# Kernel optimization log

Hardware: AMD Instinct MI355X
Metric: run time of the kernel (lower is better)

Reference implementation:

```python
import jax, jax.numpy as jnp
import numpy as np

N_NODES = 50000
N_GRAPHS = 32
NODE_F = 16
GLOBAL_F = 2
HID = 300
LAT = 100
N_EDGES = 800000


def _glorot(key, shape):
    fan_in, fan_out = shape[0], shape[1]
    s = jnp.sqrt(2.0 / (fan_in + fan_out))
    return jax.random.normal(key, shape, dtype=jnp.float32) * s


def setup_inputs() -> dict:
    key = jax.random.key(0)
    ks = jax.random.split(key, 24)
    x = jax.random.normal(ks[0], (N_NODES, NODE_F), dtype=jnp.float32)
    edge_index = jax.random.randint(ks[1], (2, N_EDGES), 0, N_NODES, dtype=jnp.int64)
    batch = jnp.sort(jax.random.randint(ks[2], (N_NODES,), 0, N_GRAPHS, dtype=jnp.int64))
    u = jax.random.normal(ks[3], (N_GRAPHS, GLOBAL_F), dtype=jnp.float32)
    # layer 0: in=NODE_F, layer 1: in=LAT
    p = {}
    p['l0_w1'] = _glorot(ks[4], (2 * NODE_F, HID)); p['l0_b1'] = jnp.zeros((HID,), jnp.float32)
    p['l0_w2'] = _glorot(ks[5], (HID, HID));        p['l0_b2'] = jnp.zeros((HID,), jnp.float32)
    p['l0_w3'] = _glorot(ks[6], (HID, LAT));        p['l0_b3'] = jnp.zeros((LAT,), jnp.float32)
    p['l1_w1'] = _glorot(ks[7], (2 * LAT, HID));    p['l1_b1'] = jnp.zeros((HID,), jnp.float32)
    p['l1_w2'] = _glorot(ks[8], (HID, HID));        p['l1_b2'] = jnp.zeros((HID,), jnp.float32)
    p['l1_w3'] = _glorot(ks[9], (HID, LAT));        p['l1_b3'] = jnp.zeros((LAT,), jnp.float32)
    p['lin_w1'] = _glorot(ks[10], (LAT + GLOBAL_F, LAT)); p['lin_b1'] = jnp.zeros((LAT,), jnp.float32)
    p['lin_w2'] = _glorot(ks[11], (LAT, LAT));            p['lin_b2'] = jnp.zeros((LAT,), jnp.float32)
    p['lin_w3'] = _glorot(ks[12], (LAT, 1));              p['lin_b3'] = jnp.zeros((1,), jnp.float32)
    return dict(x=x, edge_index=edge_index, batch=batch, u=u, **p)


def _edge_layer(x, src, dst, w1, b1, w2, b2, w3, b3):
    # gather endpoints; torch_geometric default flow: x_j = x[src], x_i = x[dst]
    xi = x[dst]
    xj = x[src]
    inp = jnp.concatenate([xi, xj - xi], axis=-1)          # [E, 2*in]
    h = jax.nn.relu(inp @ w1 + b1)
    h = jax.nn.relu(h @ w2 + b2)
    m = h @ w3 + b3                                         # [E, out]
    s = jax.ops.segment_sum(m, dst, num_segments=N_NODES)  # scatter-sum to target nodes
    cnt = jax.ops.segment_sum(jnp.ones((m.shape[0],), m.dtype), dst, num_segments=N_NODES)
    return s / jnp.maximum(cnt, 1.0)[:, None]               # scatter-mean


def _mean_pool(x, batch):
    s = jax.ops.segment_sum(x, batch, num_segments=N_GRAPHS)
    cnt = jax.ops.segment_sum(jnp.ones((x.shape[0],), x.dtype), batch, num_segments=N_GRAPHS)
    return s / jnp.maximum(cnt, 1.0)[:, None]


def reference(x, edge_index, batch, u,
              l0_w1, l0_b1, l0_w2, l0_b2, l0_w3, l0_b3,
              l1_w1, l1_b1, l1_w2, l1_b2, l1_w3, l1_b3,
              lin_w1, lin_b1, lin_w2, lin_b2, lin_w3, lin_b3):
    src, dst = edge_index[0], edge_index[1]
    x = _edge_layer(x, src, dst, l0_w1, l0_b1, l0_w2, l0_b2, l0_w3, l0_b3)
    x = jax.nn.relu(x)
    x = _edge_layer(x, src, dst, l1_w1, l1_b1, l1_w2, l1_b2, l1_w3, l1_b3)
    x = jax.nn.relu(x)
    pooled = jnp.concatenate([_mean_pool(x, batch), u], axis=1)  # [G, LAT+GLOBAL_F]
    h = jax.nn.relu(pooled @ lin_w1 + lin_b1)
    h = jax.nn.relu(h @ lin_w2 + lin_b2)
    return h @ lin_w3 + lin_b3  # [G, 1]
```

## Files before the change

### kernel.cpp

```cpp
#include <hip/hip_runtime.h>
#include <cstdint>
#include <cstddef>

#define N_NODES  50000
#define N_GRAPHS 32
#define NODE_F   16
#define GLOBAL_F 2
#define HID      300
#define LAT      100
#define N_EDGES  800000

#define HIDP 320
#define LATP 128
#define NCT1 (HIDP/16)
#define NCT2 (LATP/16)
#define NKS  (HIDP/32)
#define EPB  64
#define NTILE 12500
#define HSFS 132

#define W2F_ELEMS 102400
#define W3F_ELEMS 40960
#define W1F0_ELEMS 20480
#define W1F1_ELEMS 81920

typedef __bf16 bf16x8 __attribute__((ext_vector_type(8)));
typedef float  f32x4  __attribute__((ext_vector_type(4)));

__device__ __forceinline__ float relu_f(float x){ return fmaxf(x, 0.f); }

__device__ __forceinline__ unsigned short f2bf(float x){
  unsigned int u = __float_as_uint(x);
  u = (u + 0x7FFFu + ((u >> 16) & 1u)) >> 16;
  return (unsigned short)u;
}
__device__ __forceinline__ unsigned short f2bf_hw(float x){
  __bf16 h = (__bf16)x;
  return __builtin_bit_cast(unsigned short, h);
}
__device__ __forceinline__ float bf2f(unsigned int h){
  return __uint_as_float(h << 16);
}

__device__ __forceinline__ void pack_one(const float* __restrict__ w, int K, int N,
                                         int nct, unsigned short* __restrict__ out, int i){
  int j  = i & 7;
  int l  = (i >> 3) & 63;
  int t  = i >> 9;
  int ct = t % nct, ks = t / nct;
  int n = ct*16 + (l & 15);
  int k = ks*32 + ((l >> 4) << 3) + j;
  float v = (k < K && n < N) ? w[(size_t)k*N + n] : 0.f;
  out[i] = f2bf(v);
}

__device__ __forceinline__ void pack_w1_one(const float* __restrict__ w1, int F,
                                            unsigned short* __restrict__ out, int i){
  int j  = i & 7;
  int l  = (i >> 3) & 63;
  int t  = i >> 9;
  int ct = t % 40, ks = t / 40;
  int n = ct*16 + (l & 15);
  int k = ks*32 + ((l >> 4) << 3) + j;
  float v = 0.f;
  if (k < F){
    if (n < HIDP){ if (n < HID) v = w1[(size_t)k*HID + n] - w1[(size_t)(F+k)*HID + n]; }
    else { int nn = n - HIDP; if (nn < HID) v = w1[(size_t)(F+k)*HID + nn]; }
  }
  out[i] = f2bf(v);
}

#define PR_B0 (2*N_NODES*LAT + N_NODES)
#define PR_B1 (PR_B0 + 2*W2F_ELEMS + 2*W3F_ELEMS)
#define PR_B2 (PR_B1 + W1F0_ELEMS)
#define PR_B3 (PR_B2 + W1F1_ELEMS)
#define PR_B4 (PR_B3 + HIDP)
#define PR_B5 (PR_B4 + N_NODES*32)

__global__ void prep_kernel(
    int* __restrict__ zero_region,
    const float* __restrict__ w2a, const float* __restrict__ w3a,
    const float* __restrict__ w2b, const float* __restrict__ w3b,
    unsigned short* __restrict__ o2a, unsigned short* __restrict__ o3a,
    unsigned short* __restrict__ o2b, unsigned short* __restrict__ o3b,
    const float* __restrict__ w1a, unsigned short* __restrict__ o1a,
    const float* __restrict__ w1b, unsigned short* __restrict__ o1b,
    const float* __restrict__ ba0, const float* __restrict__ ba1,
    const float* __restrict__ ba2, const float* __restrict__ ba3,
    float* __restrict__ bo0, float* __restrict__ bo1,
    float* __restrict__ bo2, float* __restrict__ bo3,
    const float* __restrict__ x, unsigned short* __restrict__ xb){
  int i = blockIdx.x*blockDim.x + threadIdx.x;
  if (i < PR_B0){ zero_region[i] = 0; return; }
  if (i < PR_B1){
    int t = i - PR_B0;
    if (t < W2F_ELEMS) pack_one(w2a, HID, HID, NCT1, o2a, t);
    else if (t < W2F_ELEMS + W3F_ELEMS) pack_one(w3a, HID, LAT, NCT2, o3a, t - W2F_ELEMS);
    else if (t < 2*W2F_ELEMS + W3F_ELEMS) pack_one(w2b, HID, HID, NCT1, o2b, t - W2F_ELEMS - W3F_ELEMS);
    else pack_one(w3b, HID, LAT, NCT2, o3b, t - 2*W2F_ELEMS - W3F_ELEMS);
    return;
  }
  if (i < PR_B2){ pack_w1_one(w1a, NODE_F, o1a, i - PR_B1); return; }
  if (i < PR_B3){ pack_w1_one(w1b, LAT,    o1b, i - PR_B2); return; }
  if (i < PR_B4){
    int t = i - PR_B3;
    bo0[t] = (t < HID) ? ba0[t] : 0.f;
    bo1[t] = (t < HID) ? ba1[t] : 0.f;
    bo2[t] = (t < HID) ? ba2[t] : 0.f;
    bo3[t] = (t < HID) ? ba3[t] : 0.f;
    return;
  }
  if (i < PR_B5){
    int t = i - PR_B4;
    int n = t >> 5, c = t & 31;
    xb[t] = (c < NODE_F) ? f2bf(x[(size_t)n*NODE_F + c]) : 0;
    return;
  }
}

__global__ void hist_kernel(const int* __restrict__ ei, int* __restrict__ hist){
  int e = blockIdx.x*blockDim.x + threadIdx.x;
  if (e < N_EDGES) atomicAdd(&hist[ei[N_EDGES + e]], 1);
}

__global__ __launch_bounds__(256) void scan_kernel(const int* __restrict__ hist,
                                                   int* __restrict__ woff){
  __shared__ int part[256];
  const int t = threadIdx.x;
  const int CH = (N_NODES + 255) / 256;
  const int lo = t*CH, hi = (lo + CH < N_NODES) ? lo + CH : N_NODES;
  int s = 0;
  for (int i = lo; i < hi; ++i) s += hist[i];
  part[t] = s;
  __syncthreads();
  for (int d = 1; d < 256; d <<= 1){
    int v = (t >= d) ? part[t-d] : 0;
    __syncthreads();
    part[t] += v;
    __syncthreads();
  }
  int run = (t == 0) ? 0 : part[t-1];
  for (int i = lo; i < hi; ++i){ woff[i] = run; run += hist[i]; }
}

__global__ void sort_gstart(const int* __restrict__ ei, int* __restrict__ woff,
                            int2* __restrict__ esd,
                            const int* __restrict__ batch, int* __restrict__ gstart){
  int e = blockIdx.x*blockDim.x + threadIdx.x;
  if (e < N_EDGES){
    int s = ei[e], d = ei[N_EDGES + e];
    int pos = atomicAdd(&woff[d], 1);
    esd[pos] = make_int2(s, d);
  }
  if (e < N_NODES){
    int n = e;
    int b = batch[n];
    if (n == 0){ for (int g = 0; g <= b; ++g) gstart[g] = 0; }
    else {
      int bp = batch[n-1];
      for (int g = bp+1; g <= b; ++g) gstart[g] = n;
    }
    if (n == N_NODES-1){ for (int g = b+1; g <= N_GRAPHS; ++g) gstart[g] = N_NODES; }
  }
}

__global__ __launch_bounds__(256) void node_gemm0(
    const unsigned short* __restrict__ xb, const unsigned short* __restrict__ wf,
    const float* __restrict__ b1p,
    unsigned short* __restrict__ Ub, unsigned short* __restrict__ Vb){
  constexpr int KPAD = 32, NCH = KPAD/8;
  __shared__ __align__(16) unsigned short at[NCH][66][8];
  const int tid = threadIdx.x;
  const int n0 = blockIdx.x*64;
  for (int i = tid; i < 64*NCH; i += 256){
    int row = i / NCH, c = i % NCH;
    int n = n0 + row; if (n >= N_NODES) n = N_NODES-1;
    *(uint4*)&at[c][row][0] = *(const uint4*)&xb[(size_t)n*KPAD + c*8];
  }
  __syncthreads();
  const int wave = tid >> 6, l = tid & 63;
  const int lrow = l & 15, lq = l >> 4;
  f32x4 acc[4][10];
  #pragma unroll
  for (int rt = 0; rt < 4; ++rt)
    #pragma unroll
    for (int c = 0; c < 10; ++c)
      acc[rt][c] = (f32x4){0.f,0.f,0.f,0.f};
  for (int ks = 0; ks < KPAD/32; ++ks){
    bf16x8 a[4];
    #pragma unroll
    for (int rt = 0; rt < 4; ++rt)
      a[rt] = __builtin_bit_cast(bf16x8, *(const uint4*)&at[4*ks + lq][16*rt + lrow][0]);
    #pragma unroll
    for (int c = 0; c < 10; ++c){
      int ct = wave*10 + c;
      bf16x8 b = __builtin_bit_cast(bf16x8,
                   *(const uint4*)&wf[(((size_t)(ks*40 + ct)) << 9) + l*8]);
      #pragma unroll
      for (int rt = 0; rt < 4; ++rt)
        acc[rt][c] = __builtin_amdgcn_mfma_f32_16x16x32_bf16(a[rt], b, acc[rt][c], 0, 0, 0);
    }
  }
  #pragma unroll
  for (int c = 0; c < 10; ++c){
    int col = (wave*10 + c)*16 + lrow;
    const bool isU = (col < HIDP);
    const float bv = isU ? b1p[col] : 0.f;
    #pragma unroll
    for (int rt = 0; rt < 4; ++rt){
      #pragma unroll
      for (int r = 0; r < 4; ++r){
        int n = n0 + rt*16 + lq*4 + r;
        if (n < N_NODES){
          if (isU) Ub[(size_t)n*HIDP + col] = f2bf_hw(acc[rt][c][r] + bv);
          else     Vb[(size_t)n*HIDP + col - HIDP] = f2bf_hw(acc[rt][c][r]);
        }
      }
    }
  }
}

__global__ __launch_bounds__(256) void node_gemm1(
    const float* __restrict__ nacc, const int* __restrict__ hist,
    const float* __restrict__ b3,
    const unsigned short* __restrict__ wf, const float* __restrict__ b1p,
    unsigned short* __restrict__ Ub, unsigned short* __restrict__ Vb){
  constexpr int KPAD = 128, NCH = KPAD/8;
  __shared__ __align__(16) unsigned short at[NCH][66][8];
  const int tid = threadIdx.x;
  const int n0 = blockIdx.x*64;
  for (int i = tid; i < 64*NCH; i += 256){
    int row = i >> 4, c = i & 15;
    int n = n0 + row; if (n >= N_NODES) n = N_NODES-1;
    unsigned short o[8];
    if (c < 13){
      int cnt = hist[n];
      float inv = 1.f / fmaxf((float)cnt, 1.f);
      float4 a = *(const float4*)&nacc[(size_t)n*LAT + c*8];
      float4 b = (c < 12) ? *(const float4*)&nacc[(size_t)n*LAT + c*8 + 4]
                          : make_float4(0.f,0.f,0.f,0.f);
      float vals[8] = {a.x,a.y,a.z,a.w,b.x,b.y,b.z,b.w};
      #pragma unroll
      for (int q = 0; q < 8; ++q){
        int col = c*8 + q;
        float v = 0.f;
        if (col < LAT){
          v = vals[q]*inv + ((cnt > 0) ? b3[col] : 0.f);
          v = relu_f(v);
        }
        o[q] = f2bf_hw(v);
      }
    } else {
      #pragma unroll
      for (int q = 0; q < 8; ++q) o[q] = 0;
    }
    *(uint4*)&at[c][row][0] = *(const uint4*)o;
  }
  __syncthreads();
  const int wave = tid >> 6, l = tid & 63;
  const int lrow = l & 15, lq = l >> 4;
  f32x4 acc[4][10];
  #pragma unroll
  for (int rt = 0; rt < 4; ++rt)
    #pragma unroll
    for (int c = 0; c < 10; ++c)
      acc[rt][c] = (f32x4){0.f,0.f,0.f,0.f};
  for (int ks = 0; ks < KPAD/32; ++ks){
    bf16x8 a[4];
    #pragma unroll
    for (int rt = 0; rt < 4; ++rt)
      a[rt] = __builtin_bit_cast(bf16x8, *(const uint4*)&at[4*ks + lq][16*rt + lrow][0]);
    #pragma unroll
    for (int c = 0; c < 10; ++c){
      int ct = wave*10 + c;
      bf16x8 b = __builtin_bit_cast(bf16x8,
                   *(const uint4*)&wf[(((size_t)(ks*40 + ct)) << 9) + l*8]);
      #pragma unroll
      for (int rt = 0; rt < 4; ++rt)
        acc[rt][c] = __builtin_amdgcn_mfma_f32_16x16x32_bf16(a[rt], b, acc[rt][c], 0, 0, 0);
    }
  }
  #pragma unroll
  for (int c = 0; c < 10; ++c){
    int col = (wave*10 + c)*16 + lrow;
    const bool isU = (col < HIDP);
    const float bv = isU ? b1p[col] : 0.f;
    #pragma unroll
    for (int rt = 0; rt < 4; ++rt){
      #pragma unroll
      for (int r = 0; r < 4; ++r){
        int n = n0 + rt*16 + lq*4 + r;
        if (n < N_NODES){
          if (isU) Ub[(size_t)n*HIDP + col] = f2bf_hw(acc[rt][c][r] + bv);
          else     Vb[(size_t)n*HIDP + col - HIDP] = f2bf_hw(acc[rt][c][r]);
        }
      }
    }
  }
}

__global__ __launch_bounds__(256, 3) void edge_mfma(
    const int2* __restrict__ esd,
    const unsigned short* __restrict__ U, const unsigned short* __restrict__ V,
    const unsigned short* __restrict__ w2f,
    const float* __restrict__ b2p, const unsigned short* __restrict__ w3f,
    float* __restrict__ nodeacc){
  __shared__ __align__(16) unsigned short hsb[40*64*8];
  __shared__ int sdst[EPB];
  __shared__ int sflag[EPB];
  float* hsf = (float*)hsb;
  #define HS(c,row) (hsb + (((((c)<<6)) + (((row) ^ (((c)&3)<<2)))) << 3))

  const int tid = threadIdx.x;
  const int bid = blockIdx.x;
  const int rtile = (bid & 7)*1563 + (bid >> 3);
  if (rtile >= NTILE) return;
  const int e0 = rtile * EPB;
  const int eL = tid & 63;
  const int2 se = esd[e0 + eL];
  const int mysrc = se.x, mydst = se.y;
  if (tid < EPB) sdst[tid] = mydst;

  const size_t ub = (size_t)mydst*HIDP;
  const size_t vb = (size_t)mysrc*HIDP;
  const int c0 = tid >> 6;
  uint4 uu = *(const uint4*)&U[ub + c0*8];
  uint4 vv = *(const uint4*)&V[vb + c0*8];
  #pragma unroll
  for (int it = 0; it < 10; ++it){
    const int c = c0 + it*4;
    uint4 uun, vvn;
    if (it < 9){
      uun = *(const uint4*)&U[ub + (size_t)(c+4)*8];
      vvn = *(const uint4*)&V[vb + (size_t)(c+4)*8];
    }
    const unsigned int ua[4] = {uu.x,uu.y,uu.z,uu.w};
    const unsigned int va[4] = {vv.x,vv.y,vv.z,vv.w};
    unsigned int ou[4];
    #pragma unroll
    for (int q = 0; q < 4; ++q){
      float f0 = relu_f(bf2f(ua[q] & 0xFFFFu) + bf2f(va[q] & 0xFFFFu));
      float f1 = relu_f(bf2f(ua[q] >> 16)     + bf2f(va[q] >> 16));
      ou[q] = (unsigned int)f2bf_hw(f0) | ((unsigned int)f2bf_hw(f1) << 16);
    }
    *(uint4*)HS(c, eL) = make_uint4(ou[0], ou[1], ou[2], ou[3]);
    if (it < 9){ uu = uun; vv = vvn; }
  }
  __syncthreads();

  const int wave = tid >> 6, l = tid & 63;
  const int lrow = l & 15, lq = l >> 4;

  f32x4 acc1[4][5];
  #pragma unroll
  for (int rt = 0; rt < 4; ++rt)
    #pragma unroll
    for (int c = 0; c < 5; ++c)
      acc1[rt][c] = (f32x4){0.f,0.f,0.f,0.f};
  for (int ks = 0; ks < NKS; ++ks){
    bf16x8 a[4];
    #pragma unroll
    for (int rt = 0; rt < 4; ++rt)
      a[rt] = __builtin_bit_cast(bf16x8, *(const uint4*)HS(4*ks + lq, 16*rt + lrow));
    #pragma unroll
    for (int c = 0; c < 5; ++c){
      int ct = wave*5 + c;
      bf16x8 b = __builtin_bit_cast(bf16x8,
                   *(const uint4*)&w2f[(((size_t)(ks*NCT1 + ct)) << 9) + l*8]);
      #pragma unroll
      for (int rt = 0; rt < 4; ++rt)
        acc1[rt][c] = __builtin_amdgcn_mfma_f32_16x16x32_bf16(a[rt], b, acc1[rt][c], 0, 0, 0);
    }
  }
  __syncthreads();

  #pragma unroll
  for (int c = 0; c < 5; ++c){
    int col = (wave*5 + c)*16 + lrow;
    float b2v = b2p[col];
    #pragma unroll
    for (int rt = 0; rt < 4; ++rt){
      #pragma unroll
      for (int r = 0; r < 4; ++r){
        int row = rt*16 + lq*4 + r;
        HS(col >> 3, row)[col & 7] = f2bf_hw(relu_f(acc1[rt][c][r] + b2v));
      }
    }
  }
  __syncthreads();

  f32x4 acc2[4][2];
  #pragma unroll
  for (int rt = 0; rt < 4; ++rt)
    #pragma unroll
    for (int c = 0; c < 2; ++c)
      acc2[rt][c] = (f32x4){0.f,0.f,0.f,0.f};
  for (int ks = 0; ks < NKS; ++ks){
    bf16x8 a[4];
    #pragma unroll
    for (int rt = 0; rt < 4; ++rt)
      a[rt] = __builtin_bit_cast(bf16x8, *(const uint4*)HS(4*ks + lq, 16*rt + lrow));
    #pragma unroll
    for (int c = 0; c < 2; ++c){
      int ct = wave*2 + c;
      bf16x8 b = __builtin_bit_cast(bf16x8,
                   *(const uint4*)&w3f[(((size_t)(ks*NCT2 + ct)) << 9) + l*8]);
      #pragma unroll
      for (int rt = 0; rt < 4; ++rt)
        acc2[rt][c] = __builtin_amdgcn_mfma_f32_16x16x32_bf16(a[rt], b, acc2[rt][c], 0, 0, 0);
    }
  }
  __syncthreads();

  #pragma unroll
  for (int c = 0; c < 2; ++c){
    int col = (wave*2 + c)*16 + lrow;
    #pragma unroll
    for (int rt = 0; rt < 4; ++rt){
      #pragma unroll
      for (int r = 0; r < 4; ++r){
        int row = rt*16 + lq*4 + r;
        hsf[row*HSFS + col] = acc2[rt][c][r];
      }
    }
  }
  if (tid < EPB) sflag[tid] = (tid == 0) || (sdst[tid] != sdst[tid-1]);
  __syncthreads();

  {
    const int col = tid & 127;
    if (col < LAT){
      for (int s = tid >> 7; s < EPB; s += 2){
        if (!sflag[s]) continue;
        int d = sdst[s];
        float sum = hsf[s*HSFS + col];
        int r = s + 1;
        while (r < EPB && !sflag[r]){ sum += hsf[r*HSFS + col]; ++r; }
        atomicAdd(&nodeacc[(size_t)d*LAT + col], sum);
      }
    }
  }
  #undef HS
}

__global__ void finalize_kernel(const float* __restrict__ nodeacc,
                                const int* __restrict__ hist,
                                const float* __restrict__ b3,
                                unsigned short* __restrict__ x1b){
  int idx = blockIdx.x*blockDim.x + threadIdx.x;
  if (idx < N_NODES*128){
    int n = idx >> 7, j = idx & 127;
    unsigned short o = 0;
    if (j < LAT){
      int c = hist[n];
      float v = nodeacc[(size_t)n*LAT + j] / fmaxf((float)c, 1.f);
      v += (c > 0) ? b3[j] : 0.f;
      o = f2bf_hw(relu_f(v));
    }
    x1b[idx] = o;
  }
}

__global__ __launch_bounds__(1024) void pool_seg(const unsigned short* __restrict__ x1b,
                                                 const int* __restrict__ gstart,
                                                 float* __restrict__ pooled){
  __shared__ float buf[7][128];
  const int g = blockIdx.x;
  const int lo = gstart[g], hi = gstart[g+1];
  const int col = threadIdx.x & 127, q = threadIdx.x >> 7;
  float s = 0.f;
  for (int n = lo + q; n < hi; n += 8) s += bf2f(x1b[(size_t)n*128 + col]);
  if (q) buf[q-1][col] = s;
  __syncthreads();
  if (q == 0 && col < LAT){
    float tot = s;
    #pragma unroll
    for (int k = 0; k < 7; ++k) tot += buf[k][col];
    pooled[g*LAT + col] = tot / fmaxf((float)(hi - lo), 1.f);
  }
}

__global__ __launch_bounds__(128) void head_kernel(
    const float* __restrict__ pooled,
    const float* __restrict__ u,
    const float* __restrict__ w1, const float* __restrict__ bb1,
    const float* __restrict__ w2, const float* __restrict__ bb2,
    const float* __restrict__ w3, const float* __restrict__ bb3,
    float* __restrict__ out){
  __shared__ float p[N_GRAPHS][LAT+GLOBAL_F];
  __shared__ float h1[N_GRAPHS][LAT];
  __shared__ float h2[N_GRAPHS][LAT];
  const int tid = threadIdx.x;
  for (int t = tid; t < N_GRAPHS*LAT; t += 128){
    int g = t / LAT, k = t - g*LAT;
    p[g][k] = pooled[t];
  }
  for (int t = tid; t < N_GRAPHS*GLOBAL_F; t += 128){
    int g = t / GLOBAL_F, c = t - g*GLOBAL_F;
    p[g][LAT + c] = u[t];
  }
  __syncthreads();
  for (int t = tid; t < N_GRAPHS*LAT; t += 128){
    int g = t / LAT, j = t - g*LAT;
    float s = bb1[j];
    for (int k = 0; k < LAT+GLOBAL_F; k++) s += p[g][k]*w1[(size_t)k*LAT + j];
    h1[g][j] = relu_f(s);
  }
  __syncthreads();
  for (int t = tid; t < N_GRAPHS*LAT; t += 128){
    int g = t / LAT, j = t - g*LAT;
    float s = bb2[j];
    for (int k = 0; k < LAT; k++) s += h1[g][k]*w2[(size_t)k*LAT + j];
    h2[g][j] = relu_f(s);
  }
  __syncthreads();
  for (int t = tid; t < N_GRAPHS; t += 128){
    float s = bb3[0];
    for (int k = 0; k < LAT; k++) s += h2[t][k]*w3[k];
    out[t] = s;
  }
}

extern "C" void kernel_launch(void* const* d_in, const int* in_sizes, int n_in,
                              void* d_out, int out_size, void* d_ws, size_t ws_size,
                              hipStream_t stream){
  (void)in_sizes; (void)n_in; (void)out_size; (void)ws_size;
  const float* x     = (const float*)d_in[0];
  const int*   ei    = (const int*)d_in[1];
  const int*   batch = (const int*)d_in[2];
  const float* u     = (const float*)d_in[3];
  const float* l0_w1 = (const float*)d_in[4];  const float* l0_b1 = (const float*)d_in[5];
  const float* l0_w2 = (const float*)d_in[6];  const float* l0_b2 = (const float*)d_in[7];
  const float* l0_w3 = (const float*)d_in[8];  const float* l0_b3 = (const float*)d_in[9];
  const float* l1_w1 = (const float*)d_in[10]; const float* l1_b1 = (const float*)d_in[11];
  const float* l1_w2 = (const float*)d_in[12]; const float* l1_b2 = (const float*)d_in[13];
  const float* l1_w3 = (const float*)d_in[14]; const float* l1_b3 = (const float*)d_in[15];
  const float* lin_w1= (const float*)d_in[16]; const float* lin_b1= (const float*)d_in[17];
  const float* lin_w2= (const float*)d_in[18]; const float* lin_b2= (const float*)d_in[19];
  const float* lin_w3= (const float*)d_in[20]; const float* lin_b3= (const float*)d_in[21];

  char* wsb = (char*)d_ws;
  const size_t UV_BYTES = (size_t)N_NODES*HIDP*sizeof(unsigned short);

  unsigned short* Ub   = (unsigned short*)wsb;  wsb += UV_BYTES;
  unsigned short* Vb   = (unsigned short*)wsb;  wsb += UV_BYTES;
  unsigned short* w2f0 = (unsigned short*)wsb;  wsb += (size_t)W2F_ELEMS*2;
  unsigned short* w3f0 = (unsigned short*)wsb;  wsb += (size_t)W3F_ELEMS*2;
  unsigned short* w2f1 = (unsigned short*)wsb;  wsb += (size_t)W2F_ELEMS*2;
  unsigned short* w3f1 = (unsigned short*)wsb;  wsb += (size_t)W3F_ELEMS*2;
  unsigned short* w1f0 = (unsigned short*)wsb;  wsb += (size_t)W1F0_ELEMS*2;
  unsigned short* w1f1 = (unsigned short*)wsb;  wsb += (size_t)W1F1_ELEMS*2;
  float* b1p0 = (float*)wsb;                    wsb += HIDP*4;
  float* b2p0 = (float*)wsb;                    wsb += HIDP*4;
  float* b1p1 = (float*)wsb;                    wsb += HIDP*4;
  float* b2p1 = (float*)wsb;                    wsb += HIDP*4;
  unsigned short* xb0 = (unsigned short*)wsb;   wsb += (size_t)N_NODES*32*2;
  unsigned short* x1b = (unsigned short*)wsb;   wsb += (size_t)N_NODES*128*2;
  float* nodeaccA = (float*)wsb;                wsb += (size_t)N_NODES*LAT*4;
  float* nodeaccB = (float*)wsb;                wsb += (size_t)N_NODES*LAT*4;
  int*   hist    = (int*)wsb;                   wsb += (size_t)N_NODES*4;
  int*   woff    = (int*)wsb;                   wsb += (size_t)N_NODES*4;
  int2*  esd     = (int2*)wsb;                  wsb += (size_t)N_EDGES*8;
  int*   gstart  = (int*)wsb;                   wsb += 64*4;
  float* pooled  = (float*)wsb;                 wsb += (size_t)N_GRAPHS*LAT*4;

  hipLaunchKernelGGL(prep_kernel, dim3((PR_B5+255)/256), dim3(256), 0, stream,
                     (int*)nodeaccA,
                     l0_w2, l0_w3, l1_w2, l1_w3, w2f0, w3f0, w2f1, w3f1,
                     l0_w1, w1f0, l1_w1, w1f1,
                     l0_b1, l0_b2, l1_b1, l1_b2, b1p0, b2p0, b1p1, b2p1,
                     x, xb0);
  hipLaunchKernelGGL(hist_kernel, dim3((N_EDGES+255)/256), dim3(256), 0, stream, ei, hist);
  hipLaunchKernelGGL(scan_kernel, dim3(1), dim3(256), 0, stream, hist, woff);
  hipLaunchKernelGGL(sort_gstart, dim3((N_EDGES+255)/256), dim3(256), 0, stream,
                     ei, woff, esd, batch, gstart);

  const int NGB = (N_NODES + 63)/64;
  const int NEBP = 8*1563;

  hipLaunchKernelGGL(node_gemm0, dim3(NGB), dim3(256), 0, stream,
                     xb0, w1f0, b1p0, Ub, Vb);
  hipLaunchKernelGGL(edge_mfma, dim3(NEBP), dim3(256), 0, stream,
                     esd, Ub, Vb, w2f0, b2p0, w3f0, nodeaccA);

  hipLaunchKernelGGL(node_gemm1, dim3(NGB), dim3(256), 0, stream,
                     nodeaccA, hist, l0_b3, w1f1, b1p1, Ub, Vb);
  hipLaunchKernelGGL(edge_mfma, dim3(NEBP), dim3(256), 0, stream,
                     esd, Ub, Vb, w2f1, b2p1, w3f1, nodeaccB);
  hipLaunchKernelGGL(finalize_kernel, dim3((N_NODES*128+255)/256), dim3(256), 0, stream,
                     nodeaccB, hist, l1_b3, x1b);

  hipLaunchKernelGGL(pool_seg, dim3(N_GRAPHS), dim3(1024), 0, stream, x1b, gstart, pooled);
  hipLaunchKernelGGL(head_kernel, dim3(1), dim3(128), 0, stream,
                     pooled, u, lin_w1, lin_b1, lin_w2, lin_b2, lin_w3, lin_b3,
                     (float*)d_out);
}
```

Baseline: 1.558 ms.

## Switch bf16 MFMA path to fp16, reuse one node accumulator, simplify edge tiling

Moves all packed weights, activations and MFMA calls from bf16 to fp16. The edge prologue now does add and relu as packed half-vector ops instead of per-element unpack, convert and repack. The two node accumulator buffers become one, with node_gemm1 zeroing it after reading, which shrinks the prep zero-fill. The edge kernel drops its interleaved tile remap in favour of a plain blockIdx mapping. Using fp16 narrows the dynamic range of intermediates compared with bf16, and the plain mapping changes the order in which scatter atomics hit memory.

```diff
diff --git a/kernel.cpp b/kernel.cpp
--- a/kernel.cpp
+++ b/kernel.cpp
@@ -24,22 +24,17 @@
 #define W1F0_ELEMS 20480
 #define W1F1_ELEMS 81920
 
-typedef __bf16 bf16x8 __attribute__((ext_vector_type(8)));
-typedef float  f32x4  __attribute__((ext_vector_type(4)));
+typedef _Float16 f16x8 __attribute__((ext_vector_type(8)));
+typedef float    f32x4 __attribute__((ext_vector_type(4)));
 
 __device__ __forceinline__ float relu_f(float x){ return fmaxf(x, 0.f); }
 
-__device__ __forceinline__ unsigned short f2bf(float x){
-  unsigned int u = __float_as_uint(x);
-  u = (u + 0x7FFFu + ((u >> 16) & 1u)) >> 16;
-  return (unsigned short)u;
-}
-__device__ __forceinline__ unsigned short f2bf_hw(float x){
-  __bf16 h = (__bf16)x;
+__device__ __forceinline__ unsigned short f2h(float x){
+  _Float16 h = (_Float16)x;
   return __builtin_bit_cast(unsigned short, h);
 }
-__device__ __forceinline__ float bf2f(unsigned int h){
-  return __uint_as_float(h << 16);
+__device__ __forceinline__ float h2f(unsigned short v){
+  return (float)__builtin_bit_cast(_Float16, v);
 }
 
 __device__ __forceinline__ void pack_one(const float* __restrict__ w, int K, int N,
@@ -51,7 +46,7 @@
   int n = ct*16 + (l & 15);
   int k = ks*32 + ((l >> 4) << 3) + j;
   float v = (k < K && n < N) ? w[(size_t)k*N + n] : 0.f;
-  out[i] = f2bf(v);
+  out[i] = f2h(v);
 }
 
 __device__ __forceinline__ void pack_w1_one(const float* __restrict__ w1, int F,
@@ -67,10 +62,10 @@
     if (n < HIDP){ if (n < HID) v = w1[(size_t)k*HID + n] - w1[(size_t)(F+k)*HID + n]; }
     else { int nn = n - HIDP; if (nn < HID) v = w1[(size_t)(F+k)*HID + nn]; }
   }
-  out[i] = f2bf(v);
-}
-
-#define PR_B0 (2*N_NODES*LAT + N_NODES)
+  out[i] = f2h(v);
+}
+
+#define PR_B0 (N_NODES*LAT + N_NODES)
 #define PR_B1 (PR_B0 + 2*W2F_ELEMS + 2*W3F_ELEMS)
 #define PR_B2 (PR_B1 + W1F0_ELEMS)
 #define PR_B3 (PR_B2 + W1F1_ELEMS)
@@ -113,7 +108,7 @@
   if (i < PR_B5){
     int t = i - PR_B4;
     int n = t >> 5, c = t & 31;
-    xb[t] = (c < NODE_F) ? f2bf(x[(size_t)n*NODE_F + c]) : 0;
+    xb[t] = (c < NODE_F) ? f2h(x[(size_t)n*NODE_F + c]) : 0;
     return;
   }
 }
@@ -187,18 +182,18 @@
     for (int c = 0; c < 10; ++c)
       acc[rt][c] = (f32x4){0.f,0.f,0.f,0.f};
   for (int ks = 0; ks < KPAD/32; ++ks){
-    bf16x8 a[4];
+    f16x8 a[4];
     #pragma unroll
     for (int rt = 0; rt < 4; ++rt)
-      a[rt] = __builtin_bit_cast(bf16x8, *(const uint4*)&at[4*ks + lq][16*rt + lrow][0]);
+      a[rt] = __builtin_bit_cast(f16x8, *(const uint4*)&at[4*ks + lq][16*rt + lrow][0]);
     #pragma unroll
     for (int c = 0; c < 10; ++c){
       int ct = wave*10 + c;
-      bf16x8 b = __builtin_bit_cast(bf16x8,
+      f16x8 b = __builtin_bit_cast(f16x8,
                    *(const uint4*)&wf[(((size_t)(ks*40 + ct)) << 9) + l*8]);
       #pragma unroll
       for (int rt = 0; rt < 4; ++rt)
-        acc[rt][c] = __builtin_amdgcn_mfma_f32_16x16x32_bf16(a[rt], b, acc[rt][c], 0, 0, 0);
+        acc[rt][c] = __builtin_amdgcn_mfma_f32_16x16x32_f16(a[rt], b, acc[rt][c], 0, 0, 0);
     }
   }
   #pragma unroll
@@ -212,8 +207,8 @@
       for (int r = 0; r < 4; ++r){
         int n = n0 + rt*16 + lq*4 + r;
         if (n < N_NODES){
-          if (isU) Ub[(size_t)n*HIDP + col] = f2bf_hw(acc[rt][c][r] + bv);
-          else     Vb[(size_t)n*HIDP + col - HIDP] = f2bf_hw(acc[rt][c][r]);
+          if (isU) Ub[(size_t)n*HIDP + col] = f2h(acc[rt][c][r] + bv);
+          else     Vb[(size_t)n*HIDP + col - HIDP] = f2h(acc[rt][c][r]);
         }
       }
     }
@@ -221,7 +216,7 @@
 }
 
 __global__ __launch_bounds__(256) void node_gemm1(
-    const float* __restrict__ nacc, const int* __restrict__ hist,
+    float* __restrict__ nacc, const int* __restrict__ hist,
     const float* __restrict__ b3,
     const unsigned short* __restrict__ wf, const float* __restrict__ b1p,
     unsigned short* __restrict__ Ub, unsigned short* __restrict__ Vb){
@@ -231,11 +226,14 @@
   const int n0 = blockIdx.x*64;
   for (int i = tid; i < 64*NCH; i += 256){
     int row = i >> 4, c = i & 15;
-    int n = n0 + row; if (n >= N_NODES) n = N_NODES-1;
+    int nr = n0 + row;
+    const bool owner = (nr < N_NODES);
+    int n = owner ? nr : N_NODES-1;
     unsigned short o[8];
     if (c < 13){
       int cnt = hist[n];
       float inv = 1.f / fmaxf((float)cnt, 1.f);
+      float bsel = (cnt > 0) ? 1.f : 0.f;
       float4 a = *(const float4*)&nacc[(size_t)n*LAT + c*8];
       float4 b = (c < 12) ? *(const float4*)&nacc[(size_t)n*LAT + c*8 + 4]
                           : make_float4(0.f,0.f,0.f,0.f);
@@ -244,11 +242,12 @@
       for (int q = 0; q < 8; ++q){
         int col = c*8 + q;
         float v = 0.f;
-        if (col < LAT){
-          v = vals[q]*inv + ((cnt > 0) ? b3[col] : 0.f);
-          v = relu_f(v);
-        }
-        o[q] = f2bf_hw(v);
+        if (col < LAT) v = relu_f(vals[q]*inv + bsel*b3[col]);
+        o[q] = f2h(v);
+      }
+      if (owner){
+        *(float4*)&nacc[(size_t)n*LAT + c*8] = make_float4(0.f,0.f,0.f,0.f);
+        if (c < 12) *(float4*)&nacc[(size_t)n*LAT + c*8 + 4] = make_float4(0.f,0.f,0.f,0.f);
       }
     } else {
       #pragma unroll
@@ -266,18 +265,18 @@
     for (int c = 0; c < 10; ++c)
       acc[rt][c] = (f32x4){0.f,0.f,0.f,0.f};
   for (int ks = 0; ks < KPAD/32; ++ks){
-    bf16x8 a[4];
+    f16x8 a[4];
     #pragma unroll
     for (int rt = 0; rt < 4; ++rt)
-      a[rt] = __builtin_bit_cast(bf16x8, *(const uint4*)&at[4*ks + lq][16*rt + lrow][0]);
+      a[rt] = __builtin_bit_cast(f16x8, *(const uint4*)&at[4*ks + lq][16*rt + lrow][0]);
     #pragma unroll
     for (int c = 0; c < 10; ++c){
       int ct = wave*10 + c;
-      bf16x8 b = __builtin_bit_cast(bf16x8,
+      f16x8 b = __builtin_bit_cast(f16x8,
                    *(const uint4*)&wf[(((size_t)(ks*40 + ct)) << 9) + l*8]);
       #pragma unroll
       for (int rt = 0; rt < 4; ++rt)
-        acc[rt][c] = __builtin_amdgcn_mfma_f32_16x16x32_bf16(a[rt], b, acc[rt][c], 0, 0, 0);
+        acc[rt][c] = __builtin_amdgcn_mfma_f32_16x16x32_f16(a[rt], b, acc[rt][c], 0, 0, 0);
     }
   }
   #pragma unroll
@@ -291,8 +290,8 @@
       for (int r = 0; r < 4; ++r){
         int n = n0 + rt*16 + lq*4 + r;
         if (n < N_NODES){
-          if (isU) Ub[(size_t)n*HIDP + col] = f2bf_hw(acc[rt][c][r] + bv);
-          else     Vb[(size_t)n*HIDP + col - HIDP] = f2bf_hw(acc[rt][c][r]);
+          if (isU) Ub[(size_t)n*HIDP + col] = f2h(acc[rt][c][r] + bv);
+          else     Vb[(size_t)n*HIDP + col - HIDP] = f2h(acc[rt][c][r]);
         }
       }
     }
@@ -312,10 +311,7 @@
   #define HS(c,row) (hsb + (((((c)<<6)) + (((row) ^ (((c)&3)<<2)))) << 3))
 
   const int tid = threadIdx.x;
-  const int bid = blockIdx.x;
-  const int rtile = (bid & 7)*1563 + (bid >> 3);
-  if (rtile >= NTILE) return;
-  const int e0 = rtile * EPB;
+  const int e0 = blockIdx.x * EPB;
   const int eL = tid & 63;
   const int2 se = esd[e0 + eL];
   const int mysrc = se.x, mydst = se.y;
@@ -326,6 +322,7 @@
   const int c0 = tid >> 6;
   uint4 uu = *(const uint4*)&U[ub + c0*8];
   uint4 vv = *(const uint4*)&V[vb + c0*8];
+  const f16x8 zero8 = (f16x8)(_Float16)0.f;
   #pragma unroll
   for (int it = 0; it < 10; ++it){
     const int c = c0 + it*4;
@@ -334,16 +331,9 @@
       uun = *(const uint4*)&U[ub + (size_t)(c+4)*8];
       vvn = *(const uint4*)&V[vb + (size_t)(c+4)*8];
     }
-    const unsigned int ua[4] = {uu.x,uu.y,uu.z,uu.w};
-    const unsigned int va[4] = {vv.x,vv.y,vv.z,vv.w};
-    unsigned int ou[4];
-    #pragma unroll
-    for (int q = 0; q < 4; ++q){
-      float f0 = relu_f(bf2f(ua[q] & 0xFFFFu) + bf2f(va[q] & 0xFFFFu));
-      float f1 = relu_f(bf2f(ua[q] >> 16)     + bf2f(va[q] >> 16));
-      ou[q] = (unsigned int)f2bf_hw(f0) | ((unsigned int)f2bf_hw(f1) << 16);
-    }
-    *(uint4*)HS(c, eL) = make_uint4(ou[0], ou[1], ou[2], ou[3]);
+    f16x8 s = __builtin_bit_cast(f16x8, uu) + __builtin_bit_cast(f16x8, vv);
+    s = __builtin_elementwise_max(s, zero8);
+    *(uint4*)HS(c, eL) = __builtin_bit_cast(uint4, s);
     if (it < 9){ uu = uun; vv = vvn; }
   }
   __syncthreads();
@@ -358,18 +348,18 @@
     for (int c = 0; c < 5; ++c)
       acc1[rt][c] = (f32x4){0.f,0.f,0.f,0.f};
   for (int ks = 0; ks < NKS; ++ks){
-    bf16x8 a[4];
+    f16x8 a[4];
     #pragma unroll
     for (int rt = 0; rt < 4; ++rt)
-      a[rt] = __builtin_bit_cast(bf16x8, *(const uint4*)HS(4*ks + lq, 16*rt + lrow));
+      a[rt] = __builtin_bit_cast(f16x8, *(const uint4*)HS(4*ks + lq, 16*rt + lrow));
     #pragma unroll
     for (int c = 0; c < 5; ++c){
       int ct = wave*5 + c;
-      bf16x8 b = __builtin_bit_cast(bf16x8,
+      f16x8 b = __builtin_bit_cast(f16x8,
                    *(const uint4*)&w2f[(((size_t)(ks*NCT1 + ct)) << 9) + l*8]);
       #pragma unroll
       for (int rt = 0; rt < 4; ++rt)
-        acc1[rt][c] = __builtin_amdgcn_mfma_f32_16x16x32_bf16(a[rt], b, acc1[rt][c], 0, 0, 0);
+        acc1[rt][c] = __builtin_amdgcn_mfma_f32_16x16x32_f16(a[rt], b, acc1[rt][c], 0, 0, 0);
     }
   }
   __syncthreads();
@@ -383,7 +373,7 @@
       #pragma unroll
       for (int r = 0; r < 4; ++r){
         int row = rt*16 + lq*4 + r;
-        HS(col >> 3, row)[col & 7] = f2bf_hw(relu_f(acc1[rt][c][r] + b2v));
+        HS(col >> 3, row)[col & 7] = f2h(relu_f(acc1[rt][c][r] + b2v));
       }
     }
   }
@@ -396,18 +386,18 @@
     for (int c = 0; c < 2; ++c)
       acc2[rt][c] = (f32x4){0.f,0.f,0.f,0.f};
   for (int ks = 0; ks < NKS; ++ks){
-    bf16x8 a[4];
+    f16x8 a[4];
     #pragma unroll
     for (int rt = 0; rt < 4; ++rt)
-      a[rt] = __builtin_bit_cast(bf16x8, *(const uint4*)HS(4*ks + lq, 16*rt + lrow));
+      a[rt] = __builtin_bit_cast(f16x8, *(const uint4*)HS(4*ks + lq, 16*rt + lrow));
     #pragma unroll
     for (int c = 0; c < 2; ++c){
       int ct = wave*2 + c;
-      bf16x8 b = __builtin_bit_cast(bf16x8,
+      f16x8 b = __builtin_bit_cast(f16x8,
                    *(const uint4*)&w3f[(((size_t)(ks*NCT2 + ct)) << 9) + l*8]);
       #pragma unroll
       for (int rt = 0; rt < 4; ++rt)
-        acc2[rt][c] = __builtin_amdgcn_mfma_f32_16x16x32_bf16(a[rt], b, acc2[rt][c], 0, 0, 0);
+        acc2[rt][c] = __builtin_amdgcn_mfma_f32_16x16x32_f16(a[rt], b, acc2[rt][c], 0, 0, 0);
     }
   }
   __syncthreads();
@@ -455,7 +445,7 @@
       int c = hist[n];
       float v = nodeacc[(size_t)n*LAT + j] / fmaxf((float)c, 1.f);
       v += (c > 0) ? b3[j] : 0.f;
-      o = f2bf_hw(relu_f(v));
+      o = f2h(relu_f(v));
     }
     x1b[idx] = o;
   }
@@ -469,7 +459,7 @@
   const int lo = gstart[g], hi = gstart[g+1];
   const int col = threadIdx.x & 127, q = threadIdx.x >> 7;
   float s = 0.f;
-  for (int n = lo + q; n < hi; n += 8) s += bf2f(x1b[(size_t)n*128 + col]);
+  for (int n = lo + q; n < hi; n += 8) s += h2f(x1b[(size_t)n*128 + col]);
   if (q) buf[q-1][col] = s;
   __syncthreads();
   if (q == 0 && col < LAT){
@@ -556,8 +546,7 @@
   float* b2p1 = (float*)wsb;                    wsb += HIDP*4;
   unsigned short* xb0 = (unsigned short*)wsb;   wsb += (size_t)N_NODES*32*2;
   unsigned short* x1b = (unsigned short*)wsb;   wsb += (size_t)N_NODES*128*2;
-  float* nodeaccA = (float*)wsb;                wsb += (size_t)N_NODES*LAT*4;
-  float* nodeaccB = (float*)wsb;                wsb += (size_t)N_NODES*LAT*4;
+  float* nodeacc = (float*)wsb;                 wsb += (size_t)N_NODES*LAT*4;
   int*   hist    = (int*)wsb;                   wsb += (size_t)N_NODES*4;
   int*   woff    = (int*)wsb;                   wsb += (size_t)N_NODES*4;
   int2*  esd     = (int2*)wsb;                  wsb += (size_t)N_EDGES*8;
@@ -565,7 +554,7 @@
   float* pooled  = (float*)wsb;                 wsb += (size_t)N_GRAPHS*LAT*4;
 
   hipLaunchKernelGGL(prep_kernel, dim3((PR_B5+255)/256), dim3(256), 0, stream,
-                     (int*)nodeaccA,
+                     (int*)nodeacc,
                      l0_w2, l0_w3, l1_w2, l1_w3, w2f0, w3f0, w2f1, w3f1,
                      l0_w1, w1f0, l1_w1, w1f1,
                      l0_b1, l0_b2, l1_b1, l1_b2, b1p0, b2p0, b1p1, b2p1,
@@ -576,19 +565,18 @@
                      ei, woff, esd, batch, gstart);
 
   const int NGB = (N_NODES + 63)/64;
-  const int NEBP = 8*1563;
 
   hipLaunchKernelGGL(node_gemm0, dim3(NGB), dim3(256), 0, stream,
                      xb0, w1f0, b1p0, Ub, Vb);
-  hipLaunchKernelGGL(edge_mfma, dim3(NEBP), dim3(256), 0, stream,
-                     esd, Ub, Vb, w2f0, b2p0, w3f0, nodeaccA);
+  hipLaunchKernelGGL(edge_mfma, dim3(NTILE), dim3(256), 0, stream,
+                     esd, Ub, Vb, w2f0, b2p0, w3f0, nodeacc);
 
   hipLaunchKernelGGL(node_gemm1, dim3(NGB), dim3(256), 0, stream,
-                     nodeaccA, hist, l0_b3, w1f1, b1p1, Ub, Vb);
-  hipLaunchKernelGGL(edge_mfma, dim3(NEBP), dim3(256), 0, stream,
-                     esd, Ub, Vb, w2f1, b2p1, w3f1, nodeaccB);
+                     nodeacc, hist, l0_b3, w1f1, b1p1, Ub, Vb);
+  hipLaunchKernelGGL(edge_mfma, dim3(NTILE), dim3(256), 0, stream,
+                     esd, Ub, Vb, w2f1, b2p1, w3f1, nodeacc);
   hipLaunchKernelGGL(finalize_kernel, dim3((N_NODES*128+255)/256), dim3(256), 0, stream,
-                     nodeaccB, hist, l1_b3, x1b);
+                     nodeacc, hist, l1_b3, x1b);
 
   hipLaunchKernelGGL(pool_seg, dim3(N_GRAPHS), dim3(1024), 0, stream, x1b, gstart, pooled);
   hipLaunchKernelGGL(head_kernel, dim3(1), dim3(128), 0, stream,
```

Result: slower. 1.727 ms (+10.8%).

## Reuse one node accumulator, fuse finalize into pooling, simplify edge kernel

Applied to the files above, without the earlier changes.

Both layers now share a single node accumulator: node_gemm1 zeroes each row after reading it, so prep zeroes only one buffer. The finalize and pool kernels are replaced by a 256-block partial pooling kernel that applies mean, bias and ReLU directly from the accumulator, and the head kernel sums the partials. The edge kernel drops its tile-swizzled block order, its XOR LDS swizzle (now a padded row stride) and its software-prefetched gather. The scan uses 1024 threads. Together these cut memory traffic and kernel launches, at some risk of LDS bank conflicts and lost gather overlap in the edge kernel.

```diff
diff --git a/kernel.cpp b/kernel.cpp
--- a/kernel.cpp
+++ b/kernel.cpp
@@ -17,6 +17,7 @@
 #define NKS  (HIDP/32)
 #define EPB  64
 #define NTILE 12500
+#define ROWP 66
 #define HSFS 132
 
 #define W2F_ELEMS 102400
@@ -70,7 +71,7 @@
   out[i] = f2bf(v);
 }
 
-#define PR_B0 (2*N_NODES*LAT + N_NODES)
+#define PR_B0 (N_NODES*LAT + N_NODES)
 #define PR_B1 (PR_B0 + 2*W2F_ELEMS + 2*W3F_ELEMS)
 #define PR_B2 (PR_B1 + W1F0_ELEMS)
 #define PR_B3 (PR_B2 + W1F1_ELEMS)
@@ -123,17 +124,17 @@
   if (e < N_EDGES) atomicAdd(&hist[ei[N_EDGES + e]], 1);
 }
 
-__global__ __launch_bounds__(256) void scan_kernel(const int* __restrict__ hist,
-                                                   int* __restrict__ woff){
-  __shared__ int part[256];
+__global__ __launch_bounds__(1024) void scan_kernel(const int* __restrict__ hist,
+                                                    int* __restrict__ woff){
+  __shared__ int part[1024];
   const int t = threadIdx.x;
-  const int CH = (N_NODES + 255) / 256;
+  const int CH = (N_NODES + 1023) / 1024;
   const int lo = t*CH, hi = (lo + CH < N_NODES) ? lo + CH : N_NODES;
   int s = 0;
   for (int i = lo; i < hi; ++i) s += hist[i];
   part[t] = s;
   __syncthreads();
-  for (int d = 1; d < 256; d <<= 1){
+  for (int d = 1; d < 1024; d <<= 1){
     int v = (t >= d) ? part[t-d] : 0;
     __syncthreads();
     part[t] += v;
@@ -221,7 +222,7 @@
 }
 
 __global__ __launch_bounds__(256) void node_gemm1(
-    const float* __restrict__ nacc, const int* __restrict__ hist,
+    float* __restrict__ nacc, const int* __restrict__ hist,
     const float* __restrict__ b3,
     const unsigned short* __restrict__ wf, const float* __restrict__ b1p,
     unsigned short* __restrict__ Ub, unsigned short* __restrict__ Vb){
@@ -231,11 +232,14 @@
   const int n0 = blockIdx.x*64;
   for (int i = tid; i < 64*NCH; i += 256){
     int row = i >> 4, c = i & 15;
-    int n = n0 + row; if (n >= N_NODES) n = N_NODES-1;
+    int nr = n0 + row;
+    const bool owner = (nr < N_NODES);
+    int n = owner ? nr : N_NODES-1;
     unsigned short o[8];
     if (c < 13){
       int cnt = hist[n];
       float inv = 1.f / fmaxf((float)cnt, 1.f);
+      float bsel = (cnt > 0) ? 1.f : 0.f;
       float4 a = *(const float4*)&nacc[(size_t)n*LAT + c*8];
       float4 b = (c < 12) ? *(const float4*)&nacc[(size_t)n*LAT + c*8 + 4]
                           : make_float4(0.f,0.f,0.f,0.f);
@@ -244,11 +248,12 @@
       for (int q = 0; q < 8; ++q){
         int col = c*8 + q;
         float v = 0.f;
-        if (col < LAT){
-          v = vals[q]*inv + ((cnt > 0) ? b3[col] : 0.f);
-          v = relu_f(v);
-        }
+        if (col < LAT) v = relu_f(vals[q]*inv + bsel*b3[col]);
         o[q] = f2bf_hw(v);
+      }
+      if (owner){
+        *(float4*)&nacc[(size_t)n*LAT + c*8] = make_float4(0.f,0.f,0.f,0.f);
+        if (c < 12) *(float4*)&nacc[(size_t)n*LAT + c*8 + 4] = make_float4(0.f,0.f,0.f,0.f);
       }
     } else {
       #pragma unroll
@@ -305,17 +310,14 @@
     const unsigned short* __restrict__ w2f,
     const float* __restrict__ b2p, const unsigned short* __restrict__ w3f,
     float* __restrict__ nodeacc){
-  __shared__ __align__(16) unsigned short hsb[40*64*8];
+  __shared__ __align__(16) unsigned short hsb[(HIDP/8)*ROWP*8];
   __shared__ int sdst[EPB];
   __shared__ int sflag[EPB];
   float* hsf = (float*)hsb;
-  #define HS(c,row) (hsb + (((((c)<<6)) + (((row) ^ (((c)&3)<<2)))) << 3))
+  #define HS(c,row) (hsb + (((c)*ROWP + (row)) << 3))
 
   const int tid = threadIdx.x;
-  const int bid = blockIdx.x;
-  const int rtile = (bid & 7)*1563 + (bid >> 3);
-  if (rtile >= NTILE) return;
-  const int e0 = rtile * EPB;
+  const int e0 = blockIdx.x * EPB;
   const int eL = tid & 63;
   const int2 se = esd[e0 + eL];
   const int mysrc = se.x, mydst = se.y;
@@ -323,19 +325,13 @@
 
   const size_t ub = (size_t)mydst*HIDP;
   const size_t vb = (size_t)mysrc*HIDP;
-  const int c0 = tid >> 6;
-  uint4 uu = *(const uint4*)&U[ub + c0*8];
-  uint4 vv = *(const uint4*)&V[vb + c0*8];
   #pragma unroll
   for (int it = 0; it < 10; ++it){
-    const int c = c0 + it*4;
-    uint4 uun, vvn;
-    if (it < 9){
-      uun = *(const uint4*)&U[ub + (size_t)(c+4)*8];
-      vvn = *(const uint4*)&V[vb + (size_t)(c+4)*8];
-    }
-    const unsigned int ua[4] = {uu.x,uu.y,uu.z,uu.w};
-    const unsigned int va[4] = {vv.x,vv.y,vv.z,vv.w};
+    int c = (tid + it*256) >> 6;
+    const uint4 uu = *(const uint4*)&U[ub + c*8];
+    const uint4 vv = *(const uint4*)&V[vb + c*8];
+    const unsigned int ua[4] = {uu.x, uu.y, uu.z, uu.w};
+    const unsigned int va[4] = {vv.x, vv.y, vv.z, vv.w};
     unsigned int ou[4];
     #pragma unroll
     for (int q = 0; q < 4; ++q){
@@ -344,7 +340,6 @@
       ou[q] = (unsigned int)f2bf_hw(f0) | ((unsigned int)f2bf_hw(f1) << 16);
     }
     *(uint4*)HS(c, eL) = make_uint4(ou[0], ou[1], ou[2], ou[3]);
-    if (it < 9){ uu = uun; vv = vvn; }
   }
   __syncthreads();
 
@@ -443,45 +438,31 @@
   #undef HS
 }
 
-__global__ void finalize_kernel(const float* __restrict__ nodeacc,
-                                const int* __restrict__ hist,
-                                const float* __restrict__ b3,
-                                unsigned short* __restrict__ x1b){
-  int idx = blockIdx.x*blockDim.x + threadIdx.x;
-  if (idx < N_NODES*128){
-    int n = idx >> 7, j = idx & 127;
-    unsigned short o = 0;
-    if (j < LAT){
-      int c = hist[n];
-      float v = nodeacc[(size_t)n*LAT + j] / fmaxf((float)c, 1.f);
-      v += (c > 0) ? b3[j] : 0.f;
-      o = f2bf_hw(relu_f(v));
-    }
-    x1b[idx] = o;
-  }
-}
-
-__global__ __launch_bounds__(1024) void pool_seg(const unsigned short* __restrict__ x1b,
-                                                 const int* __restrict__ gstart,
-                                                 float* __restrict__ pooled){
-  __shared__ float buf[7][128];
-  const int g = blockIdx.x;
+__global__ __launch_bounds__(256) void pool_partial(
+    const float* __restrict__ nodeacc, const int* __restrict__ hist,
+    const float* __restrict__ b3, const int* __restrict__ gstart,
+    float* __restrict__ partial){
+  __shared__ float buf[128];
+  const int g = blockIdx.x >> 3, sl = blockIdx.x & 7;
   const int lo = gstart[g], hi = gstart[g+1];
   const int col = threadIdx.x & 127, q = threadIdx.x >> 7;
   float s = 0.f;
-  for (int n = lo + q; n < hi; n += 8) s += bf2f(x1b[(size_t)n*128 + col]);
-  if (q) buf[q-1][col] = s;
-  __syncthreads();
-  if (q == 0 && col < LAT){
-    float tot = s;
-    #pragma unroll
-    for (int k = 0; k < 7; ++k) tot += buf[k][col];
-    pooled[g*LAT + col] = tot / fmaxf((float)(hi - lo), 1.f);
-  }
+  if (col < LAT){
+    const float bcol = b3[col];
+    for (int n = lo + sl*2 + q; n < hi; n += 16){
+      int cnt = hist[n];
+      float v = nodeacc[(size_t)n*LAT + col] / fmaxf((float)cnt, 1.f);
+      v += (cnt > 0) ? bcol : 0.f;
+      s += relu_f(v);
+    }
+  }
+  if (q) buf[col] = s;
+  __syncthreads();
+  if (q == 0) partial[((size_t)g*8 + sl)*128 + col] = s + buf[col];
 }
 
 __global__ __launch_bounds__(128) void head_kernel(
-    const float* __restrict__ pooled,
+    const float* __restrict__ partial, const int* __restrict__ gstart,
     const float* __restrict__ u,
     const float* __restrict__ w1, const float* __restrict__ bb1,
     const float* __restrict__ w2, const float* __restrict__ bb2,
@@ -493,7 +474,11 @@
   const int tid = threadIdx.x;
   for (int t = tid; t < N_GRAPHS*LAT; t += 128){
     int g = t / LAT, k = t - g*LAT;
-    p[g][k] = pooled[t];
+    float s = 0.f;
+    #pragma unroll
+    for (int sl = 0; sl < 8; ++sl) s += partial[((size_t)g*8 + sl)*128 + k];
+    float cnt = (float)(gstart[g+1] - gstart[g]);
+    p[g][k] = s / fmaxf(cnt, 1.f);
   }
   for (int t = tid; t < N_GRAPHS*GLOBAL_F; t += 128){
     int g = t / GLOBAL_F, c = t - g*GLOBAL_F;
@@ -555,43 +540,39 @@
   float* b1p1 = (float*)wsb;                    wsb += HIDP*4;
   float* b2p1 = (float*)wsb;                    wsb += HIDP*4;
   unsigned short* xb0 = (unsigned short*)wsb;   wsb += (size_t)N_NODES*32*2;
-  unsigned short* x1b = (unsigned short*)wsb;   wsb += (size_t)N_NODES*128*2;
-  float* nodeaccA = (float*)wsb;                wsb += (size_t)N_NODES*LAT*4;
-  float* nodeaccB = (float*)wsb;                wsb += (size_t)N_NODES*LAT*4;
+  float* nodeacc = (float*)wsb;                 wsb += (size_t)N_NODES*LAT*4;
   int*   hist    = (int*)wsb;                   wsb += (size_t)N_NODES*4;
   int*   woff    = (int*)wsb;                   wsb += (size_t)N_NODES*4;
   int2*  esd     = (int2*)wsb;                  wsb += (size_t)N_EDGES*8;
   int*   gstart  = (int*)wsb;                   wsb += 64*4;
-  float* pooled  = (float*)wsb;                 wsb += (size_t)N_GRAPHS*LAT*4;
+  float* partial = (float*)wsb;                 wsb += (size_t)N_GRAPHS*8*128*4;
 
   hipLaunchKernelGGL(prep_kernel, dim3((PR_B5+255)/256), dim3(256), 0, stream,
-                     (int*)nodeaccA,
+                     (int*)nodeacc,
                      l0_w2, l0_w3, l1_w2, l1_w3, w2f0, w3f0, w2f1, w3f1,
                      l0_w1, w1f0, l1_w1, w1f1,
                      l0_b1, l0_b2, l1_b1, l1_b2, b1p0, b2p0, b1p1, b2p1,
                      x, xb0);
   hipLaunchKernelGGL(hist_kernel, dim3((N_EDGES+255)/256), dim3(256), 0, stream, ei, hist);
-  hipLaunchKernelGGL(scan_kernel, dim3(1), dim3(256), 0, stream, hist, woff);
+  hipLaunchKernelGGL(scan_kernel, dim3(1), dim3(1024), 0, stream, hist, woff);
   hipLaunchKernelGGL(sort_gstart, dim3((N_EDGES+255)/256), dim3(256), 0, stream,
                      ei, woff, esd, batch, gstart);
 
   const int NGB = (N_NODES + 63)/64;
-  const int NEBP = 8*1563;
 
   hipLaunchKernelGGL(node_gemm0, dim3(NGB), dim3(256), 0, stream,
                      xb0, w1f0, b1p0, Ub, Vb);
-  hipLaunchKernelGGL(edge_mfma, dim3(NEBP), dim3(256), 0, stream,
-                     esd, Ub, Vb, w2f0, b2p0, w3f0, nodeaccA);
+  hipLaunchKernelGGL(edge_mfma, dim3(NTILE), dim3(256), 0, stream,
+                     esd, Ub, Vb, w2f0, b2p0, w3f0, nodeacc);
 
   hipLaunchKernelGGL(node_gemm1, dim3(NGB), dim3(256), 0, stream,
-                     nodeaccA, hist, l0_b3, w1f1, b1p1, Ub, Vb);
-  hipLaunchKernelGGL(edge_mfma, dim3(NEBP), dim3(256), 0, stream,
-                     esd, Ub, Vb, w2f1, b2p1, w3f1, nodeaccB);
-  hipLaunchKernelGGL(finalize_kernel, dim3((N_NODES*128+255)/256), dim3(256), 0, stream,
-                     nodeaccB, hist, l1_b3, x1b);
-
-  hipLaunchKernelGGL(pool_seg, dim3(N_GRAPHS), dim3(1024), 0, stream, x1b, gstart, pooled);
+                     nodeacc, hist, l0_b3, w1f1, b1p1, Ub, Vb);
+  hipLaunchKernelGGL(edge_mfma, dim3(NTILE), dim3(256), 0, stream,
+                     esd, Ub, Vb, w2f1, b2p1, w3f1, nodeacc);
+
+  hipLaunchKernelGGL(pool_partial, dim3(N_GRAPHS*8), dim3(256), 0, stream,
+                     nodeacc, hist, l1_b3, gstart, partial);
   hipLaunchKernelGGL(head_kernel, dim3(1), dim3(128), 0, stream,
-                     pooled, u, lin_w1, lin_b1, lin_w2, lin_b2, lin_w3, lin_b3,
+                     partial, gstart, u, lin_w1, lin_b1, lin_w2, lin_b2, lin_w3, lin_b3,
                      (float*)d_out);
 }
```

New measurement: 1.439 ms. 7.7% less time.
